# Kernel optimization log

Measured on AMD Instinct MI355X. Metric: run time of the kernel, lower is better.

The kernel has to match this reference:

```python
import jax, jax.numpy as jnp
import numpy as np

SEQ, N = 8192, 1024
W_SYN = 20.0

# ArcTan surrogate spike fn ('ArcTan', alpha=1.0, beta=10.0): forward = Heaviside
@jax.custom_vjp
def spike(x):
    return (x > 0).astype(x.dtype)

def _spike_fwd(x):
    return spike(x), x

def _spike_bwd(x, g):
    return (g * (1.0 / (1.0 + (10.0 * x) ** 2)),)

spike.defvjp(_spike_fwd, _spike_bwd)


def setup_inputs() -> dict:
    key = jax.random.key(0)
    k_in, = jax.random.split(key, 1)
    input_batch = jax.random.normal(k_in, (SEQ, N), dtype=jnp.float32)
    state = jnp.zeros((2, N), jnp.float32)  # (v, u)
    # learned params, sized per init_kwargs
    W1 = jnp.eye(N, dtype=jnp.float32) * W_SYN          # f1.ff.weight [N, N]
    W2 = jnp.ones((1, N), jnp.float32) * W_SYN          # f2.ff.weight [1, N]
    a = jnp.full((N,), 0.02, jnp.float32)
    b = jnp.full((N,), 0.2, jnp.float32)
    c = jnp.full((N,), -65.0, jnp.float32)
    d = jnp.full((N,), 8.0, jnp.float32)
    thresh = jnp.full((N,), 30.0, jnp.float32)
    dt = jnp.full((N,), 1.0, jnp.float32)               # time_step per neuron
    leak = jnp.full((1,), 0.99, jnp.float32)            # decode leak
    return dict(input_batch=input_batch, state=state, W1=W1, W2=W2,
                a=a, b=b, c=c, d=d, thresh=thresh, dt=dt, leak=leak)


def reference(input_batch, state, W1, W2, a, b, c, d, thresh, dt, leak):
    v0, u0 = state[0], state[1]
    dm0 = jnp.zeros((1,), input_batch.dtype)  # decode_mempot starts at 0

    def step(carry, x_t):
        v, u, dm = carry
        I = W1 @ x_t  # synaptic current [N]
        # Izhikevich ODE (Euler step)
        v_new = v + dt * (0.04 * v * v + 5.0 * v + 140.0 - u + I)
        u_new = u + dt * a * (b * v - u)
        s = spike(v_new - thresh)
        v_out = v_new * (1.0 - s) + c * s   # reset v -> c on spike
        u_out = u_new + d * s               # u -> u + d on spike
        dm_new = leak * dm + W2 @ s         # leaky-integrator decode [1]
        return (v_out, u_out, dm_new), (s, jnp.stack([v_out, u_out]), dm_new)

    _, (outputs, states, decoded) = jax.lax.scan(step, (v0, u0, dm0), input_batch)
    return outputs, states, decoded  # [T,N], [T,2,N], [T,1]
```

## Files before the change

### kernel.cpp

```cpp
#include <hip/hip_runtime.h>

#define CAP 32
#define K 32

__global__ void sparsify_kernel(const float* __restrict__ W1, int N,
                                int* __restrict__ cnts, int* __restrict__ cols,
                                float* __restrict__ wts) {
  __shared__ int scnt;
  const int row = blockIdx.x;
  if (threadIdx.x == 0) scnt = 0;
  __syncthreads();
  const float* wr = W1 + (long)row * N;
  for (int k = threadIdx.x; k < N; k += blockDim.x) {
    float w = wr[k];
    if (w != 0.0f) {
      int slot = atomicAdd(&scnt, 1);
      if (slot < CAP) {
        cols[row * CAP + slot] = k;
        wts[row * CAP + slot] = w;
      }
    }
  }
  __syncthreads();
  if (threadIdx.x == 0) {
    cnts[row] = scnt;
    if (scnt == 0) { cols[row * CAP] = 0; wts[row * CAP] = 0.0f; }
  }
}

__global__ void touch_kernel(const float4* __restrict__ x4, long n4,
                             float* __restrict__ dump) {
  long i = (long)blockIdx.x * blockDim.x + threadIdx.x;
  const long stride = (long)gridDim.x * blockDim.x;
  float acc = 0.f;
  for (; i < n4; i += stride) {
    float4 v = x4[i];
    acc += v.x + v.y + v.z + v.w;
  }
  if (acc == 1234.56789f) dump[blockIdx.x & 1023] = acc;
}

__global__ void __launch_bounds__(256) izh_pc3_kernel(
    const float* __restrict__ X, const float* __restrict__ state,
    const float* __restrict__ a, const float* __restrict__ b,
    const float* __restrict__ c, const float* __restrict__ d,
    const float* __restrict__ th, const float* __restrict__ dtv,
    const float* __restrict__ W1,
    const int* __restrict__ cnts, const int* __restrict__ cols,
    const float* __restrict__ wts,
    float* __restrict__ o_s, float* __restrict__ o_st,
    int T, int N)
{
#pragma clang fp contract(off)
  __shared__ float ibuf[2][K][64];
  __shared__ float obuf[2][K][2][64];
  __shared__ int s_fast;

  const int wid  = threadIdx.x >> 6;
  const int lane = threadIdx.x & 63;
  const int base = blockIdx.x * 64;
  const int gn   = base + lane;
  const long N2  = 2L * N;
  const int B    = T / K;

  if (wid == 0) {
    bool elig = (base + 64 <= N);
    if (elig) elig = (cnts[gn] == 1) && (dtv[gn] == 1.0f);
    unsigned long long m = __ballot(elig);
    if (lane == 0) s_fast = (m == ~0ULL) ? 1 : 0;
  }
  __syncthreads();

  if (s_fast) {
    if (wid == 1) {
      const float wn = wts[gn * CAP];
      const int   c0 = cols[gn * CAP];
      const float* Xp = X + c0;
      float xr[K];
#pragma unroll
      for (int i = 0; i < K; ++i) xr[i] = Xp[(size_t)i * N];
#pragma unroll
      for (int i = 0; i < K; ++i) ibuf[0][i][lane] = wn * xr[i];
    }
    __syncthreads();

    if (wid == 0) {
      float v = state[gn], u = state[N + gn];
      const float bn = b[gn], cn = c[gn], dn = d[gn], thn = th[gn];
      const float Pn = dtv[gn] * a[gn];

      for (int k = 0; k < B; ++k) {
        const int bsel = k & 1;
#pragma unroll
        for (int i = 0; i < K; ++i) {
          const float I = ibuf[bsel][i][lane];
          float t1 = 0.04f * v;
          float t2 = t1 * v;
          float t3 = 5.0f * v;
          float t4 = t2 + t3;
          float t5 = t4 + 140.0f;
          float t6 = t5 - u;
          float t7 = t6 + I;
          float vn = v + t7;
          float q1 = bn * v;
          float q2 = q1 - u;
          float q3 = Pn * q2;
          float un = u + q3;
          obuf[bsel][i][0][lane] = vn;
          obuf[bsel][i][1][lane] = un;
          bool sp = vn > thn;
          v = sp ? cn : vn;
          u = un + (sp ? dn : 0.0f);
        }
        asm volatile("s_waitcnt lgkmcnt(0)" ::: "memory");
        __builtin_amdgcn_s_barrier();
      }

      if (B * K < T) {
        const float w0 = wts[gn * CAP];
        const float* Xp = X + cols[gn * CAP];
        for (int t = B * K; t < T; ++t) {
          const float I = w0 * Xp[(size_t)t * N];
          float t1 = 0.04f * v; float t2 = t1 * v; float t3 = 5.0f * v;
          float t4 = t2 + t3; float t5 = t4 + 140.0f; float t6 = t5 - u;
          float t7 = t6 + I; float vn = v + t7;
          float q1 = bn * v; float q2 = q1 - u; float q3 = Pn * q2;
          float un = u + q3;
          bool sp = vn > thn;
          v = sp ? cn : vn; u = un + (sp ? dn : 0.0f);
          o_s[(long)t * N + gn] = sp ? 1.0f : 0.0f;
          o_st[(long)t * N2 + gn] = v;
          o_st[(long)t * N2 + N + gn] = u;
        }
      }
    } else if (wid == 1) {
      const float wn = wts[gn * CAP];
      const int   c0 = cols[gn * CAP];
      const float* Xp = X + c0;
      const int r = lane >> 4, j = lane & 15;
      const float4 th4 = *(const float4*)&th[base + 4 * j];

      for (int k = 0; k < B; ++k) {
        if (k + 1 < B) {
          float xr[K];
#pragma unroll
          for (int i = 0; i < K; ++i) xr[i] = Xp[(size_t)((k + 1) * K + i) * N];
#pragma unroll
          for (int i = 0; i < K; ++i) ibuf[(k + 1) & 1][i][lane] = wn * xr[i];
        }
        if (k > 0) {
          const int q = k - 1, bsel = q & 1, t0 = q * K;
#pragma unroll
          for (int i = 0; i < K; i += 4) {
            float4 vn4 = *(const float4*)&obuf[bsel][i + r][0][4 * j];
            float4 s4;
            s4.x = vn4.x > th4.x ? 1.0f : 0.0f;
            s4.y = vn4.y > th4.y ? 1.0f : 0.0f;
            s4.z = vn4.z > th4.z ? 1.0f : 0.0f;
            s4.w = vn4.w > th4.w ? 1.0f : 0.0f;
            *(float4*)(o_s + (size_t)(t0 + i + r) * N + base + 4 * j) = s4;
          }
        }
        asm volatile("s_waitcnt lgkmcnt(0)" ::: "memory");
        __builtin_amdgcn_s_barrier();
      }
      if (B > 0) {
        const int q = B - 1, bsel = q & 1, t0 = q * K;
#pragma unroll
        for (int i = 0; i < K; i += 4) {
          float4 vn4 = *(const float4*)&obuf[bsel][i + r][0][4 * j];
          float4 s4;
          s4.x = vn4.x > th4.x ? 1.0f : 0.0f;
          s4.y = vn4.y > th4.y ? 1.0f : 0.0f;
          s4.z = vn4.z > th4.z ? 1.0f : 0.0f;
          s4.w = vn4.w > th4.w ? 1.0f : 0.0f;
          *(float4*)(o_s + (size_t)(t0 + i + r) * N + base + 4 * j) = s4;
        }
      }
    } else if (wid == 2) {
      const int r = lane >> 4, j = lane & 15;
      const float4 th4 = *(const float4*)&th[base + 4 * j];
      const float4 c4  = *(const float4*)&c[base + 4 * j];

      for (int k = 0; k < B; ++k) {
        if (k > 0) {
          const int q = k - 1, bsel = q & 1, t0 = q * K;
#pragma unroll
          for (int i = 0; i < K; i += 4) {
            float4 vn4 = *(const float4*)&obuf[bsel][i + r][0][4 * j];
            float4 o4;
            o4.x = vn4.x > th4.x ? c4.x : vn4.x;
            o4.y = vn4.y > th4.y ? c4.y : vn4.y;
            o4.z = vn4.z > th4.z ? c4.z : vn4.z;
            o4.w = vn4.w > th4.w ? c4.w : vn4.w;
            *(float4*)(o_st + (size_t)(t0 + i + r) * N2 + base + 4 * j) = o4;
          }
        }
        __builtin_amdgcn_s_barrier();
      }
      if (B > 0) {
        const int q = B - 1, bsel = q & 1, t0 = q * K;
#pragma unroll
        for (int i = 0; i < K; i += 4) {
          float4 vn4 = *(const float4*)&obuf[bsel][i + r][0][4 * j];
          float4 o4;
          o4.x = vn4.x > th4.x ? c4.x : vn4.x;
          o4.y = vn4.y > th4.y ? c4.y : vn4.y;
          o4.z = vn4.z > th4.z ? c4.z : vn4.z;
          o4.w = vn4.w > th4.w ? c4.w : vn4.w;
          *(float4*)(o_st + (size_t)(t0 + i + r) * N2 + base + 4 * j) = o4;
        }
      }
    } else {
      const int r = lane >> 4, j = lane & 15;
      const float4 th4 = *(const float4*)&th[base + 4 * j];
      const float4 d4  = *(const float4*)&d[base + 4 * j];

      for (int k = 0; k < B; ++k) {
        if (k > 0) {
          const int q = k - 1, bsel = q & 1, t0 = q * K;
#pragma unroll
          for (int i = 0; i < K; i += 4) {
            float4 vn4 = *(const float4*)&obuf[bsel][i + r][0][4 * j];
            float4 un4 = *(const float4*)&obuf[bsel][i + r][1][4 * j];
            float4 o4;
            o4.x = un4.x + (vn4.x > th4.x ? d4.x : 0.0f);
            o4.y = un4.y + (vn4.y > th4.y ? d4.y : 0.0f);
            o4.z = un4.z + (vn4.z > th4.z ? d4.z : 0.0f);
            o4.w = un4.w + (vn4.w > th4.w ? d4.w : 0.0f);
            *(float4*)(o_st + (size_t)(t0 + i + r) * N2 + N + base + 4 * j) = o4;
          }
        }
        __builtin_amdgcn_s_barrier();
      }
      if (B > 0) {
        const int q = B - 1, bsel = q & 1, t0 = q * K;
#pragma unroll
        for (int i = 0; i < K; i += 4) {
          float4 vn4 = *(const float4*)&obuf[bsel][i + r][0][4 * j];
          float4 un4 = *(const float4*)&obuf[bsel][i + r][1][4 * j];
          float4 o4;
          o4.x = un4.x + (vn4.x > th4.x ? d4.x : 0.0f);
          o4.y = un4.y + (vn4.y > th4.y ? d4.y : 0.0f);
          o4.z = un4.z + (vn4.z > th4.z ? d4.z : 0.0f);
          o4.w = un4.w + (vn4.w > th4.w ? d4.w : 0.0f);
          *(float4*)(o_st + (size_t)(t0 + i + r) * N2 + N + base + 4 * j) = o4;
        }
      }
    }
  } else {
    if (wid != 0 || gn >= N) return;
    float v = state[gn], u = state[N + gn];
    const float an = a[gn], bn = b[gn], cn = c[gn], dn = d[gn];
    const float thn = th[gn], dtn = dtv[gn];
    const float Pn = dtn * an;
    const int cnt = cnts[gn];
    for (int t = 0; t < T; ++t) {
      float I = 0.0f;
      if (cnt <= CAP) {
        for (int j = 0; j < cnt; ++j)
          I = I + wts[gn * CAP + j] * X[(size_t)t * N + cols[gn * CAP + j]];
      } else {
        const float* wr = W1 + (size_t)gn * N;
        const float* xr = X + (size_t)t * N;
        for (int kk = 0; kk < N; ++kk) I = I + wr[kk] * xr[kk];
      }
      float t1 = 0.04f * v; float t2 = t1 * v; float t3 = 5.0f * v;
      float t4 = t2 + t3; float t5 = t4 + 140.0f; float t6 = t5 - u;
      float t7 = t6 + I; float t8 = dtn * t7; float vn = v + t8;
      float q1 = bn * v; float q2 = q1 - u; float q3 = Pn * q2; float un = u + q3;
      float df = vn - thn; bool sp = df > 0.0f;
      v = sp ? cn : vn; u = un + (sp ? dn : 0.0f);
      o_s[(size_t)t * N + gn] = sp ? 1.0f : 0.0f;
      o_st[(size_t)t * N2 + gn] = v;
      o_st[(size_t)t * N2 + N + gn] = u;
    }
  }
}

__global__ void decode_dot_kernel(const float* __restrict__ o_s,
                                  const float* __restrict__ W2,
                                  float* __restrict__ r, int N) {
  const int t = blockIdx.x;
  const float* srow = o_s + (long)t * N;
  float p = 0.0f;
  for (int n = threadIdx.x; n < N; n += blockDim.x)
    p += W2[n] * srow[n];
  for (int off = 32; off > 0; off >>= 1) p += __shfl_down(p, off);
  __shared__ float red[4];
  if ((threadIdx.x & 63) == 0) red[threadIdx.x >> 6] = p;
  __syncthreads();
  if (threadIdx.x == 0) {
    float tot = 0.f;
    const int nw = blockDim.x >> 6;
    for (int w = 0; w < nw; ++w) tot += red[w];
    r[t] = tot;
  }
}

__global__ void decode_scan_kernel(const float* __restrict__ r,
                                   const float* __restrict__ leakp,
                                   float* __restrict__ out, int T) {
  __shared__ float Bsh[64], Ssh[64];
  const float leakv = leakp[0];
  const int i = threadIdx.x;
  const int chunk = (T + 63) / 64;
  const int t0 = i * chunk;
  float B = 0.0f;
  for (int j = 0; j < chunk; ++j) {
    int t = t0 + j;
    if (t < T) B = leakv * B + r[t];
  }
  Bsh[i] = B;
  float A = 1.0f, p = leakv; int e = chunk;
  while (e) { if (e & 1) A *= p; p *= p; e >>= 1; }
  __syncthreads();
  if (i == 0) {
    float dm = 0.0f;
    for (int k = 0; k < 64; ++k) { Ssh[k] = dm; dm = A * dm + Bsh[k]; }
  }
  __syncthreads();
  float dm = Ssh[i];
  for (int j = 0; j < chunk; ++j) {
    int t = t0 + j;
    if (t < T) { dm = leakv * dm + r[t]; out[t] = dm; }
  }
}

extern "C" void kernel_launch(void* const* d_in, const int* in_sizes, int n_in,
                              void* d_out, int out_size, void* d_ws, size_t ws_size,
                              hipStream_t stream) {
  const float* X  = (const float*)d_in[0];
  const float* st = (const float*)d_in[1];
  const float* W1 = (const float*)d_in[2];
  const float* W2 = (const float*)d_in[3];
  const float* a  = (const float*)d_in[4];
  const float* b  = (const float*)d_in[5];
  const float* c  = (const float*)d_in[6];
  const float* d  = (const float*)d_in[7];
  const float* th = (const float*)d_in[8];
  const float* dt = (const float*)d_in[9];
  const float* lk = (const float*)d_in[10];
  const int N = in_sizes[4];
  const int T = in_sizes[0] / N;

  float* o_s  = (float*)d_out;
  float* o_st = o_s + (long)T * N;
  float* o_dm = o_st + 2L * (long)T * N;

  int*   cnts = (int*)d_ws;
  int*   cols = cnts + N;
  float* wts  = (float*)(cols + (long)N * CAP);
  float* rbuf = wts + (long)N * CAP;
  float* dump = rbuf + T;

  sparsify_kernel<<<N, 256, 0, stream>>>(W1, N, cnts, cols, wts);
  const long n4 = ((long)T * N) / 4;
  touch_kernel<<<1024, 256, 0, stream>>>((const float4*)X, n4, dump);
  const int nblk = (N + 63) / 64;
  izh_pc3_kernel<<<nblk, 256, 0, stream>>>(X, st, a, b, c, d, th, dt, W1,
                                           cnts, cols, wts, o_s, o_st, T, N);
  decode_dot_kernel<<<T, 256, 0, stream>>>(o_s, W2, rbuf, N);
  decode_scan_kernel<<<1, 64, 0, stream>>>(rbuf, lk, o_dm, T);
}
```

Baseline: 513.2 us.

## Fuse decode dot into Izhikevich kernel and widen LDS buffers to float4

Removes the separate decode_dot kernel that reread the full spike output. Each writer warp now reduces W2-weighted spikes with wave shuffles and atomically adds them into a zeroed per-timestep buffer. Also drops the X prefetch touch kernel and repacks the shared staging buffers as float4 so the compute warp does wider LDS reads and writes. Output stores become per-lane scalars instead of float4 transposed stores, which may cost store efficiency. Atomic float accumulation may also change summation order.

```diff
diff --git a/kernel.cpp b/kernel.cpp
--- a/kernel.cpp
+++ b/kernel.cpp
@@ -28,32 +28,26 @@
   }
 }
 
-__global__ void touch_kernel(const float4* __restrict__ x4, long n4,
-                             float* __restrict__ dump) {
-  long i = (long)blockIdx.x * blockDim.x + threadIdx.x;
-  const long stride = (long)gridDim.x * blockDim.x;
-  float acc = 0.f;
-  for (; i < n4; i += stride) {
-    float4 v = x4[i];
-    acc += v.x + v.y + v.z + v.w;
-  }
-  if (acc == 1234.56789f) dump[blockIdx.x & 1023] = acc;
-}
-
-__global__ void __launch_bounds__(256) izh_pc3_kernel(
+__global__ void zero_kernel(float* __restrict__ p, int n) {
+  int i = blockIdx.x * blockDim.x + threadIdx.x;
+  if (i < n) p[i] = 0.0f;
+}
+
+__global__ void __launch_bounds__(256) izh_b128_kernel(
     const float* __restrict__ X, const float* __restrict__ state,
     const float* __restrict__ a, const float* __restrict__ b,
     const float* __restrict__ c, const float* __restrict__ d,
     const float* __restrict__ th, const float* __restrict__ dtv,
-    const float* __restrict__ W1,
+    const float* __restrict__ W1, const float* __restrict__ W2,
     const int* __restrict__ cnts, const int* __restrict__ cols,
     const float* __restrict__ wts,
     float* __restrict__ o_s, float* __restrict__ o_st,
+    float* __restrict__ rbuf,
     int T, int N)
 {
 #pragma clang fp contract(off)
-  __shared__ float ibuf[2][K][64];
-  __shared__ float obuf[2][K][2][64];
+  __shared__ __align__(16) float4 ibuf4[2][K / 4][64];
+  __shared__ __align__(16) float4 obuf4[2][K / 2][64];
   __shared__ int s_fast;
 
   const int wid  = threadIdx.x >> 6;
@@ -80,7 +74,12 @@
 #pragma unroll
       for (int i = 0; i < K; ++i) xr[i] = Xp[(size_t)i * N];
 #pragma unroll
-      for (int i = 0; i < K; ++i) ibuf[0][i][lane] = wn * xr[i];
+      for (int q = 0; q < K / 4; ++q) {
+        float4 w;
+        w.x = wn * xr[4 * q];     w.y = wn * xr[4 * q + 1];
+        w.z = wn * xr[4 * q + 2]; w.w = wn * xr[4 * q + 3];
+        ibuf4[0][q][lane] = w;
+      }
     }
     __syncthreads();
 
@@ -92,25 +91,34 @@
       for (int k = 0; k < B; ++k) {
         const int bsel = k & 1;
 #pragma unroll
-        for (int i = 0; i < K; ++i) {
-          const float I = ibuf[bsel][i][lane];
-          float t1 = 0.04f * v;
-          float t2 = t1 * v;
-          float t3 = 5.0f * v;
-          float t4 = t2 + t3;
-          float t5 = t4 + 140.0f;
-          float t6 = t5 - u;
-          float t7 = t6 + I;
-          float vn = v + t7;
-          float q1 = bn * v;
-          float q2 = q1 - u;
-          float q3 = Pn * q2;
-          float un = u + q3;
-          obuf[bsel][i][0][lane] = vn;
-          obuf[bsel][i][1][lane] = un;
-          bool sp = vn > thn;
-          v = sp ? cn : vn;
-          u = un + (sp ? dn : 0.0f);
+        for (int i = 0; i < K; i += 4) {
+          const float4 IV = ibuf4[bsel][i >> 2][lane];
+          float vp = 0.f, up = 0.f;
+#pragma unroll
+          for (int h = 0; h < 4; ++h) {
+            const float Ival = (h == 0) ? IV.x : (h == 1) ? IV.y
+                             : (h == 2) ? IV.z : IV.w;
+            float t1 = 0.04f * v;
+            float t2 = t1 * v;
+            float t3 = 5.0f * v;
+            float t4 = t2 + t3;
+            float t5 = t4 + 140.0f;
+            float t6 = t5 - u;
+            float t7 = t6 + Ival;
+            float vn = v + t7;
+            float q1 = bn * v;
+            float q2 = q1 - u;
+            float q3 = Pn * q2;
+            float un = u + q3;
+            if ((h & 1) == 0) { vp = vn; up = un; }
+            else {
+              float4 W; W.x = vp; W.y = up; W.z = vn; W.w = un;
+              obuf4[bsel][(i + h) >> 1][lane] = W;
+            }
+            bool sp = vn > thn;
+            v = sp ? cn : vn;
+            u = un + (sp ? dn : 0.0f);
+          }
         }
         asm volatile("s_waitcnt lgkmcnt(0)" ::: "memory");
         __builtin_amdgcn_s_barrier();
@@ -119,6 +127,7 @@
       if (B * K < T) {
         const float w0 = wts[gn * CAP];
         const float* Xp = X + cols[gn * CAP];
+        const float w2n = W2[gn];
         for (int t = B * K; t < T; ++t) {
           const float I = w0 * Xp[(size_t)t * N];
           float t1 = 0.04f * v; float t2 = t1 * v; float t3 = 5.0f * v;
@@ -128,17 +137,20 @@
           float un = u + q3;
           bool sp = vn > thn;
           v = sp ? cn : vn; u = un + (sp ? dn : 0.0f);
-          o_s[(long)t * N + gn] = sp ? 1.0f : 0.0f;
+          float s_ = sp ? 1.0f : 0.0f;
+          o_s[(long)t * N + gn] = s_;
           o_st[(long)t * N2 + gn] = v;
           o_st[(long)t * N2 + N + gn] = u;
+          float pr = sp ? w2n : 0.0f;
+          for (int off = 32; off; off >>= 1) pr += __shfl_xor(pr, off);
+          if (lane == 0) atomicAdd(rbuf + t, pr);
         }
       }
     } else if (wid == 1) {
       const float wn = wts[gn * CAP];
       const int   c0 = cols[gn * CAP];
       const float* Xp = X + c0;
-      const int r = lane >> 4, j = lane & 15;
-      const float4 th4 = *(const float4*)&th[base + 4 * j];
+      const float thn = th[gn];
 
       for (int k = 0; k < B; ++k) {
         if (k + 1 < B) {
@@ -146,19 +158,20 @@
 #pragma unroll
           for (int i = 0; i < K; ++i) xr[i] = Xp[(size_t)((k + 1) * K + i) * N];
 #pragma unroll
-          for (int i = 0; i < K; ++i) ibuf[(k + 1) & 1][i][lane] = wn * xr[i];
+          for (int q = 0; q < K / 4; ++q) {
+            float4 w;
+            w.x = wn * xr[4 * q];     w.y = wn * xr[4 * q + 1];
+            w.z = wn * xr[4 * q + 2]; w.w = wn * xr[4 * q + 3];
+            ibuf4[(k + 1) & 1][q][lane] = w;
+          }
         }
         if (k > 0) {
           const int q = k - 1, bsel = q & 1, t0 = q * K;
 #pragma unroll
-          for (int i = 0; i < K; i += 4) {
-            float4 vn4 = *(const float4*)&obuf[bsel][i + r][0][4 * j];
-            float4 s4;
-            s4.x = vn4.x > th4.x ? 1.0f : 0.0f;
-            s4.y = vn4.y > th4.y ? 1.0f : 0.0f;
-            s4.z = vn4.z > th4.z ? 1.0f : 0.0f;
-            s4.w = vn4.w > th4.w ? 1.0f : 0.0f;
-            *(float4*)(o_s + (size_t)(t0 + i + r) * N + base + 4 * j) = s4;
+          for (int p = 0; p < K / 2; ++p) {
+            float4 O = obuf4[bsel][p][lane];
+            o_s[(size_t)(t0 + 2 * p) * N + gn]     = O.x > thn ? 1.0f : 0.0f;
+            o_s[(size_t)(t0 + 2 * p + 1) * N + gn] = O.z > thn ? 1.0f : 0.0f;
           }
         }
         asm volatile("s_waitcnt lgkmcnt(0)" ::: "memory");
@@ -167,33 +180,34 @@
       if (B > 0) {
         const int q = B - 1, bsel = q & 1, t0 = q * K;
 #pragma unroll
-        for (int i = 0; i < K; i += 4) {
-          float4 vn4 = *(const float4*)&obuf[bsel][i + r][0][4 * j];
-          float4 s4;
-          s4.x = vn4.x > th4.x ? 1.0f : 0.0f;
-          s4.y = vn4.y > th4.y ? 1.0f : 0.0f;
-          s4.z = vn4.z > th4.z ? 1.0f : 0.0f;
-          s4.w = vn4.w > th4.w ? 1.0f : 0.0f;
-          *(float4*)(o_s + (size_t)(t0 + i + r) * N + base + 4 * j) = s4;
+        for (int p = 0; p < K / 2; ++p) {
+          float4 O = obuf4[bsel][p][lane];
+          o_s[(size_t)(t0 + 2 * p) * N + gn]     = O.x > thn ? 1.0f : 0.0f;
+          o_s[(size_t)(t0 + 2 * p + 1) * N + gn] = O.z > thn ? 1.0f : 0.0f;
         }
       }
     } else if (wid == 2) {
-      const int r = lane >> 4, j = lane & 15;
-      const float4 th4 = *(const float4*)&th[base + 4 * j];
-      const float4 c4  = *(const float4*)&c[base + 4 * j];
+      const float thn = th[gn], cn = c[gn], w2n = W2[gn];
 
       for (int k = 0; k < B; ++k) {
         if (k > 0) {
           const int q = k - 1, bsel = q & 1, t0 = q * K;
 #pragma unroll
-          for (int i = 0; i < K; i += 4) {
-            float4 vn4 = *(const float4*)&obuf[bsel][i + r][0][4 * j];
-            float4 o4;
-            o4.x = vn4.x > th4.x ? c4.x : vn4.x;
-            o4.y = vn4.y > th4.y ? c4.y : vn4.y;
-            o4.z = vn4.z > th4.z ? c4.z : vn4.z;
-            o4.w = vn4.w > th4.w ? c4.w : vn4.w;
-            *(float4*)(o_st + (size_t)(t0 + i + r) * N2 + base + 4 * j) = o4;
+          for (int p = 0; p < K / 2; ++p) {
+            float4 O = obuf4[bsel][p][lane];
+            bool sp0 = O.x > thn, sp1 = O.z > thn;
+            o_st[(size_t)(t0 + 2 * p) * N2 + gn]     = sp0 ? cn : O.x;
+            o_st[(size_t)(t0 + 2 * p + 1) * N2 + gn] = sp1 ? cn : O.z;
+            float p0 = sp0 ? w2n : 0.0f;
+            float p1 = sp1 ? w2n : 0.0f;
+            for (int off = 32; off; off >>= 1) {
+              p0 += __shfl_xor(p0, off);
+              p1 += __shfl_xor(p1, off);
+            }
+            if (lane == 0) {
+              atomicAdd(rbuf + t0 + 2 * p, p0);
+              atomicAdd(rbuf + t0 + 2 * p + 1, p1);
+            }
           }
         }
         __builtin_amdgcn_s_barrier();
@@ -201,34 +215,36 @@
       if (B > 0) {
         const int q = B - 1, bsel = q & 1, t0 = q * K;
 #pragma unroll
-        for (int i = 0; i < K; i += 4) {
-          float4 vn4 = *(const float4*)&obuf[bsel][i + r][0][4 * j];
-          float4 o4;
-          o4.x = vn4.x > th4.x ? c4.x : vn4.x;
-          o4.y = vn4.y > th4.y ? c4.y : vn4.y;
-          o4.z = vn4.z > th4.z ? c4.z : vn4.z;
-          o4.w = vn4.w > th4.w ? c4.w : vn4.w;
-          *(float4*)(o_st + (size_t)(t0 + i + r) * N2 + base + 4 * j) = o4;
+        for (int p = 0; p < K / 2; ++p) {
+          float4 O = obuf4[bsel][p][lane];
+          bool sp0 = O.x > thn, sp1 = O.z > thn;
+          o_st[(size_t)(t0 + 2 * p) * N2 + gn]     = sp0 ? cn : O.x;
+          o_st[(size_t)(t0 + 2 * p + 1) * N2 + gn] = sp1 ? cn : O.z;
+          float p0 = sp0 ? w2n : 0.0f;
+          float p1 = sp1 ? w2n : 0.0f;
+          for (int off = 32; off; off >>= 1) {
+            p0 += __shfl_xor(p0, off);
+            p1 += __shfl_xor(p1, off);
+          }
+          if (lane == 0) {
+            atomicAdd(rbuf + t0 + 2 * p, p0);
+            atomicAdd(rbuf + t0 + 2 * p + 1, p1);
+          }
         }
       }
     } else {
-      const int r = lane >> 4, j = lane & 15;
-      const float4 th4 = *(const float4*)&th[base + 4 * j];
-      const float4 d4  = *(const float4*)&d[base + 4 * j];
+      const float thn = th[gn], dn = d[gn];
 
       for (int k = 0; k < B; ++k) {
         if (k > 0) {
           const int q = k - 1, bsel = q & 1, t0 = q * K;
 #pragma unroll
-          for (int i = 0; i < K; i += 4) {
-            float4 vn4 = *(const float4*)&obuf[bsel][i + r][0][4 * j];
-            float4 un4 = *(const float4*)&obuf[bsel][i + r][1][4 * j];
-            float4 o4;
-            o4.x = un4.x + (vn4.x > th4.x ? d4.x : 0.0f);
-            o4.y = un4.y + (vn4.y > th4.y ? d4.y : 0.0f);
-            o4.z = un4.z + (vn4.z > th4.z ? d4.z : 0.0f);
-            o4.w = un4.w + (vn4.w > th4.w ? d4.w : 0.0f);
-            *(float4*)(o_st + (size_t)(t0 + i + r) * N2 + N + base + 4 * j) = o4;
+          for (int p = 0; p < K / 2; ++p) {
+            float4 O = obuf4[bsel][p][lane];
+            o_st[(size_t)(t0 + 2 * p) * N2 + N + gn] =
+                O.y + (O.x > thn ? dn : 0.0f);
+            o_st[(size_t)(t0 + 2 * p + 1) * N2 + N + gn] =
+                O.w + (O.z > thn ? dn : 0.0f);
           }
         }
         __builtin_amdgcn_s_barrier();
@@ -236,15 +252,12 @@
       if (B > 0) {
         const int q = B - 1, bsel = q & 1, t0 = q * K;
 #pragma unroll
-        for (int i = 0; i < K; i += 4) {
-          float4 vn4 = *(const float4*)&obuf[bsel][i + r][0][4 * j];
-          float4 un4 = *(const float4*)&obuf[bsel][i + r][1][4 * j];
-          float4 o4;
-          o4.x = un4.x + (vn4.x > th4.x ? d4.x : 0.0f);
-          o4.y = un4.y + (vn4.y > th4.y ? d4.y : 0.0f);
-          o4.z = un4.z + (vn4.z > th4.z ? d4.z : 0.0f);
-          o4.w = un4.w + (vn4.w > th4.w ? d4.w : 0.0f);
-          *(float4*)(o_st + (size_t)(t0 + i + r) * N2 + N + base + 4 * j) = o4;
+        for (int p = 0; p < K / 2; ++p) {
+          float4 O = obuf4[bsel][p][lane];
+          o_st[(size_t)(t0 + 2 * p) * N2 + N + gn] =
+              O.y + (O.x > thn ? dn : 0.0f);
+          o_st[(size_t)(t0 + 2 * p + 1) * N2 + N + gn] =
+              O.w + (O.z > thn ? dn : 0.0f);
         }
       }
     }
@@ -254,6 +267,7 @@
     const float an = a[gn], bn = b[gn], cn = c[gn], dn = d[gn];
     const float thn = th[gn], dtn = dtv[gn];
     const float Pn = dtn * an;
+    const float w2n = W2[gn];
     const int cnt = cnts[gn];
     for (int t = 0; t < T; ++t) {
       float I = 0.0f;
@@ -271,30 +285,12 @@
       float q1 = bn * v; float q2 = q1 - u; float q3 = Pn * q2; float un = u + q3;
       float df = vn - thn; bool sp = df > 0.0f;
       v = sp ? cn : vn; u = un + (sp ? dn : 0.0f);
-      o_s[(size_t)t * N + gn] = sp ? 1.0f : 0.0f;
+      float s_ = sp ? 1.0f : 0.0f;
+      o_s[(size_t)t * N + gn] = s_;
       o_st[(size_t)t * N2 + gn] = v;
       o_st[(size_t)t * N2 + N + gn] = u;
+      if (s_ != 0.0f) atomicAdd(rbuf + t, w2n);
     }
-  }
-}
-
-__global__ void decode_dot_kernel(const float* __restrict__ o_s,
-                                  const float* __restrict__ W2,
-                                  float* __restrict__ r, int N) {
-  const int t = blockIdx.x;
-  const float* srow = o_s + (long)t * N;
-  float p = 0.0f;
-  for (int n = threadIdx.x; n < N; n += blockDim.x)
-    p += W2[n] * srow[n];
-  for (int off = 32; off > 0; off >>= 1) p += __shfl_down(p, off);
-  __shared__ float red[4];
-  if ((threadIdx.x & 63) == 0) red[threadIdx.x >> 6] = p;
-  __syncthreads();
-  if (threadIdx.x == 0) {
-    float tot = 0.f;
-    const int nw = blockDim.x >> 6;
-    for (int w = 0; w < nw; ++w) tot += red[w];
-    r[t] = tot;
   }
 }
 
@@ -352,14 +348,12 @@
   int*   cols = cnts + N;
   float* wts  = (float*)(cols + (long)N * CAP);
   float* rbuf = wts + (long)N * CAP;
-  float* dump = rbuf + T;
 
   sparsify_kernel<<<N, 256, 0, stream>>>(W1, N, cnts, cols, wts);
-  const long n4 = ((long)T * N) / 4;
-  touch_kernel<<<1024, 256, 0, stream>>>((const float4*)X, n4, dump);
+  zero_kernel<<<(T + 255) / 256, 256, 0, stream>>>(rbuf, T);
   const int nblk = (N + 63) / 64;
-  izh_pc3_kernel<<<nblk, 256, 0, stream>>>(X, st, a, b, c, d, th, dt, W1,
-                                           cnts, cols, wts, o_s, o_st, T, N);
-  decode_dot_kernel<<<T, 256, 0, stream>>>(o_s, W2, rbuf, N);
+  izh_b128_kernel<<<nblk, 256, 0, stream>>>(X, st, a, b, c, d, th, dt, W1, W2,
+                                            cnts, cols, wts, o_s, o_st, rbuf,
+                                            T, N);
   decode_scan_kernel<<<1, 64, 0, stream>>>(rbuf, lk, o_dm, T);
 }
```

Result: slower. 1.657 ms (+222.8%).
